# Performance work log

Measured on AMD Instinct MI355X. Metric: run time of the kernel, lower is better.

Reference implementation:

```python
import jax, jax.numpy as jnp
import numpy as np

HUMAN_EXHALATION_FLOW = 0.0052  # ENV_CONFIG.HUMAN_EXHALATION_FLOW
TIME_STEP = 1.0                 # ENV_CONFIG.TIME_STEP
N_NODES = 100_000
N_EDGES = 3_200_000
IN_DIM, OUT_DIM, K = 4, 1, 3
T_HIST = 16


def setup_inputs() -> dict:
    key = jax.random.key(0)
    k1, k2, k3, k4, k5 = jax.random.split(key, 5)
    # columns at [:, -1, :]: 0=concentration, 1=people, 2=size (size divides -> keep away from 0)
    origin_data = jax.random.uniform(k1, (N_NODES, T_HIST, 3), jnp.float32, 0.5, 1.5)
    # raw flow field: conv with kernel K (VALID) maps [E+K-1, K, IN_DIM] -> [E, 1, OUT_DIM]
    flow = jax.random.normal(k2, (N_EDGES + K - 1, K, IN_DIM), jnp.float32)
    edge_index = jax.random.randint(k3, (2, N_EDGES), 0, N_NODES, jnp.int32)
    conv_w = jax.random.normal(k4, (OUT_DIM, IN_DIM, K, K), jnp.float32) * 0.1
    conv_b = jax.random.normal(k5, (OUT_DIM,), jnp.float32) * 0.1
    return {"origin_data": origin_data, "flow": flow, "conv_w": conv_w,
            "conv_b": conv_b, "edge_index": edge_index}


def _flow_conv(flow, conv_w, conv_b):
    # [H, W, C] -> [1, C, H, W] -> conv -> [H', W', out_dim]
    x = jnp.transpose(flow, (2, 0, 1))[None]
    y = jax.lax.conv_general_dilated(
        x, conv_w, window_strides=(1, 1), padding='VALID',
        dimension_numbers=('NCHW', 'OIHW', 'NCHW'))
    y = y + conv_b[None, :, None, None]
    return jnp.transpose(y[0], (1, 2, 0))  # [E, 1, out_dim]


def reference(origin_data, flow, conv_w, conv_b, edge_index):
    concentration = origin_data[:, -1, 0]  # [N]
    people = origin_data[:, -1, 1]         # [N]
    size = origin_data[:, -1, 2]           # [N]
    n = concentration.shape[0]
    mask = jnp.ones((n,), concentration.dtype).at[-1].set(0.0)

    fc = _flow_conv(flow, conv_w, conv_b)  # [E, 1, 1]
    val = fc[:, 0, 0]                      # [E]

    src, dst = edge_index[0], edge_index[1]
    # original loop uses .item() everywhere -> these terms are detached from autodiff
    c_sg = jax.lax.stop_gradient(concentration)
    s_sg = jax.lax.stop_gradient(size)
    v_sg = jax.lax.stop_gradient(val)
    msg = jnp.where(src != dst, v_sg * c_sg[src], 0.0)  # skip self-loops
    node_new = jnp.zeros((n,), concentration.dtype)
    node_new = node_new.at[src].add(-msg / s_sg[src] * TIME_STEP)
    node_new = node_new.at[dst].add(msg / s_sg[dst] * TIME_STEP)

    exhaled = HUMAN_EXHALATION_FLOW * jax.lax.stop_gradient(people) / s_sg  # .item() loop -> detached
    result = concentration + (node_new + exhaled * TIME_STEP) * mask
    out2 = jnp.concatenate([edge_index.T.astype(val.dtype), fc[:, :, 0]], axis=1)  # [E, 3]
    return result[:, None], out2
```

## Files before the change

kernel.cpp:

```cpp
#include <hip/hip_runtime.h>


#define WSH  14
#define WSZ  16384
#define PBF  32

#define OWSH 13
#define OWSZ 8192
#define OPB  16
#define OFPS 8192.0f
#define OQBIAS (1 << 20)
#define OQCLMP ((1 << 19) - 1)

__global__ __launch_bounds__(256) void prep(
    const float* __restrict__ od,
    float* __restrict__ conc,
    unsigned long long* __restrict__ acc,
    int n_nodes)
{
    int n = blockIdx.x * blockDim.x + threadIdx.x;
    if (n >= n_nodes) return;
    conc[n] = od[(long long)n * 48 + 45];
    if (acc) acc[n] = 0ULL;
}

__global__ __launch_bounds__(256) void edge_conv(
    const float* __restrict__ flow, const int* __restrict__ ei,
    const float* __restrict__ conv_w, const float* __restrict__ conv_b,
    const float* __restrict__ conc,
    float* __restrict__ out2, float* __restrict__ bcv, int n_edges)
{
    __shared__ float w[40];
    int t = threadIdx.x;
    if (t < 36) {
        int i  = t & 3;
        int kw = (t >> 2) % 3;
        int kh = t / 12;
        w[t] = conv_w[i * 9 + kh * 3 + kw];
    }
    if (t == 36) w[36] = conv_b[0];
    __syncthreads();

    int e = blockIdx.x * blockDim.x + t;
    if (e >= n_edges) return;

    int s = ei[e];
    int d = ei[n_edges + e];
    float cs = bcv ? conc[s] : 0.0f;

    const float4* fp = (const float4*)(flow + (long long)e * 12);
    float acc = w[36];
#pragma unroll
    for (int q = 0; q < 9; ++q) {
        float4 v = fp[q];
        acc = fmaf(v.x, w[q * 4 + 0], acc);
        acc = fmaf(v.y, w[q * 4 + 1], acc);
        acc = fmaf(v.z, w[q * 4 + 2], acc);
        acc = fmaf(v.w, w[q * 4 + 3], acc);
    }

    float* o = out2 + (long long)e * 3;
    o[0] = (float)s;
    o[1] = (float)d;
    o[2] = acc;
    if (bcv) bcv[e] = acc * cs;
}

__global__ __launch_bounds__(1024) void accum_f(
    const float* __restrict__ out2,
    const float* __restrict__ bcv,
    float* __restrict__ pA,
    float* __restrict__ pB,
    int n_edges, int n_win, int stride)
{
    __shared__ float tA[WSZ];
    __shared__ float tB[WSZ];

    const int xcd = blockIdx.x & 7;
    const int i   = blockIdx.x >> 3;
    const int j   = i / n_win;
    const int sl  = xcd * (PBF >> 3) + j;
    const int w   = i - j * n_win;

    const int t = threadIdx.x;
    for (int k = t; k < WSZ; k += 1024) { tA[k] = 0.f; tB[k] = 0.f; }
    __syncthreads();

    const long long e0 = (long long)sl * n_edges / PBF;
    const long long e1 = (long long)(sl + 1) * n_edges / PBF;

#define PROC(fs, fd, vv, bb)                                          \
    {                                                                  \
        int s_ = (int)(fs), d_ = (int)(fd);                            \
        if (s_ != d_) {                                                \
            if ((s_ >> WSH) == w) atomicAdd(&tA[s_ & (WSZ - 1)], (vv));\
            if ((d_ >> WSH) == w) atomicAdd(&tB[d_ & (WSZ - 1)], (bb));\
        }                                                              \
    }

    long long e = e0 + t;
    for (; e + 3 * 1024 < e1; e += 4 * 1024) {
        const float* r  = out2 + e * 3;
        const float* bb = bcv + e;
        float fs0 = r[0],    fd0 = r[1],    v0 = r[2];
        float fs1 = r[3072], fd1 = r[3073], v1 = r[3074];
        float fs2 = r[6144], fd2 = r[6145], v2 = r[6146];
        float fs3 = r[9216], fd3 = r[9217], v3 = r[9218];
        float b0 = bb[0], b1 = bb[1024], b2 = bb[2048], b3 = bb[3072];
        PROC(fs0, fd0, v0, b0);
        PROC(fs1, fd1, v1, b1);
        PROC(fs2, fd2, v2, b2);
        PROC(fs3, fd3, v3, b3);
    }
    for (; e < e1; e += 1024) {
        const float* r = out2 + e * 3;
        float fs = r[0], fd = r[1], vv = r[2];
        float bb = bcv[e];
        PROC(fs, fd, vv, bb);
    }
#undef PROC
    __syncthreads();

    float* dA = pA + (long long)sl * stride + ((long long)w << WSH);
    float* dB = pB + (long long)sl * stride + ((long long)w << WSH);
    for (int k = t; k < (WSZ >> 2); k += 1024) {
        ((float4*)dA)[k] = ((const float4*)tA)[k];
        ((float4*)dB)[k] = ((const float4*)tB)[k];
    }
}

__global__ __launch_bounds__(256) void node_final_f(
    const float* __restrict__ od,
    const float* __restrict__ conc,
    const float* __restrict__ pA,
    const float* __restrict__ pB,
    float* __restrict__ out, int n_nodes, int stride)
{
    int n = blockIdx.x * blockDim.x + threadIdx.x;
    if (n >= n_nodes) return;

    float a0 = 0.f, a1 = 0.f, a2 = 0.f, a3 = 0.f;
    float b0 = 0.f, b1 = 0.f, b2 = 0.f, b3 = 0.f;
#pragma unroll
    for (int sl = 0; sl < PBF; sl += 4) {
        a0 += pA[(long long)(sl + 0) * stride + n];
        a1 += pA[(long long)(sl + 1) * stride + n];
        a2 += pA[(long long)(sl + 2) * stride + n];
        a3 += pA[(long long)(sl + 3) * stride + n];
        b0 += pB[(long long)(sl + 0) * stride + n];
        b1 += pB[(long long)(sl + 1) * stride + n];
        b2 += pB[(long long)(sl + 2) * stride + n];
        b3 += pB[(long long)(sl + 3) * stride + n];
    }
    float a = (a0 + a1) + (a2 + a3);
    float b = (b0 + b1) + (b2 + b3);

    long long bi = (long long)n * 48 + 45;
    float c  = conc[n];
    float p  = od[bi + 1];
    float is = 1.0f / od[bi + 2];

    float r = c;
    if (n != n_nodes - 1)
        r += (b - a * c) * is + 0.0052f * p * is;
    out[n] = r;
}

__global__ __launch_bounds__(1024) void accum_o(
    const float* __restrict__ out2,
    const float* __restrict__ conc,
    unsigned long long* __restrict__ acc,
    int n_edges, int n_nodes)
{
    __shared__ float tA[OWSZ];
    __shared__ float tB[OWSZ];

    const int w    = blockIdx.x / OPB;
    const int sl   = blockIdx.x % OPB;
    const int base = w << OWSH;

    for (int i = threadIdx.x; i < OWSZ; i += 1024) { tA[i] = 0.f; tB[i] = 0.f; }
    __syncthreads();

    const long long e0 = (long long)sl * n_edges / OPB;
    const long long e1 = (long long)(sl + 1) * n_edges / OPB;
    for (long long e = e0 + threadIdx.x; e < e1; e += 1024) {
        const float* r = out2 + e * 3;
        float fs = r[0], fd = r[1], v = r[2];
        int s = (int)fs, d = (int)fd;
        if (s == d) continue;
        if ((s >> OWSH) == w) atomicAdd(&tA[s - base], v);
        if ((d >> OWSH) == w) atomicAdd(&tB[d - base], v * conc[s]);
    }
    __syncthreads();

    for (int i = threadIdx.x; i < OWSZ; i += 1024) {
        int n = base + i;
        if (n >= n_nodes) continue;
        float a = tA[i], b = tB[i];
        if (a == 0.f && b == 0.f) continue;
        int qa = __float2int_rn(a * OFPS);
        int qb = __float2int_rn(b * OFPS);
        qa = min(max(qa, -OQCLMP), OQCLMP);
        qb = min(max(qb, -OQCLMP), OQCLMP);
        unsigned long long enc =
            ((unsigned long long)(unsigned)(qa + OQBIAS) << 37) +
            ((unsigned long long)(unsigned)(qb + OQBIAS) << 10) + 1ULL;
        atomicAdd(acc + n, enc);
    }
}

__global__ __launch_bounds__(256) void node_final_o(
    const float* __restrict__ od,
    const float* __restrict__ conc,
    const unsigned long long* __restrict__ acc,
    float* __restrict__ out, int n_nodes)
{
    int n = blockIdx.x * blockDim.x + threadIdx.x;
    if (n >= n_nodes) return;

    unsigned long long t = acc[n];
    long long cnt = (long long)(t & 1023ULL);
    unsigned long long t2 = t >> 10;
    long long sbr = (long long)(t2 & ((1ULL << 27) - 1));
    long long sar = (long long)(t2 >> 27);
    float a = (float)(sar - cnt * OQBIAS) * (1.0f / OFPS);
    float b = (float)(sbr - cnt * OQBIAS) * (1.0f / OFPS);

    long long bi = (long long)n * 48 + 45;
    float c  = conc[n];
    float p  = od[bi + 1];
    float is = 1.0f / od[bi + 2];

    float r = c;
    if (n != n_nodes - 1)
        r += (b - a * c) * is + 0.0052f * p * is;
    out[n] = r;
}

extern "C" void kernel_launch(void* const* d_in, const int* in_sizes, int n_in,
                              void* d_out, int out_size, void* d_ws, size_t ws_size,
                              hipStream_t stream) {
    const float* od   = (const float*)d_in[0];
    const float* flow = (const float*)d_in[1];
    const float* cw   = (const float*)d_in[2];
    const float* cb   = (const float*)d_in[3];
    const int*   ei   = (const int*)d_in[4];

    const int n_nodes = in_sizes[0] / 48;
    const int n_edges = in_sizes[4] / 2;

    float* out_res = (float*)d_out;
    float* out2    = out_res + n_nodes;

    dim3 blk(256);
    dim3 grid_nodes((n_nodes + 255) / 256);
    dim3 grid_edges((n_edges + 255) / 256);

    const int n_win  = (n_nodes + WSZ - 1) >> WSH;
    const int stride = n_win << WSH;
    size_t off = 0;
    size_t o_conc = off; off += (((size_t)n_nodes * 4) + 255) & ~255ULL;
    size_t o_bc   = off; off += (((size_t)n_edges * 4) + 255) & ~255ULL;
    size_t o_pA   = off; off += (((size_t)PBF * stride * 4) + 255) & ~255ULL;
    size_t o_pB   = off; off += (((size_t)PBF * stride * 4) + 255) & ~255ULL;
    const bool full = (ws_size >= off);

    float* conc = (float*)((char*)d_ws + o_conc);

    if (full) {
        float* bcv = (float*)((char*)d_ws + o_bc);
        float* pA  = (float*)((char*)d_ws + o_pA);
        float* pB  = (float*)((char*)d_ws + o_pB);

        prep<<<grid_nodes, blk, 0, stream>>>(od, conc, nullptr, n_nodes);
        edge_conv<<<grid_edges, blk, 0, stream>>>(flow, ei, cw, cb, conc,
                                                  out2, bcv, n_edges);
        accum_f<<<dim3(n_win * PBF), dim3(1024), 0, stream>>>(
            out2, bcv, pA, pB, n_edges, n_win, stride);
        node_final_f<<<grid_nodes, blk, 0, stream>>>(od, conc, pA, pB,
                                                     out_res, n_nodes, stride);
    } else {
        unsigned long long* acc =
            (unsigned long long*)((char*)d_ws + (((size_t)n_nodes * 4 + 7) / 8 * 8));
        const int n_win_o = (n_nodes + OWSZ - 1) >> OWSH;

        prep<<<grid_nodes, blk, 0, stream>>>(od, conc, acc, n_nodes);
        edge_conv<<<grid_edges, blk, 0, stream>>>(flow, ei, cw, cb, conc,
                                                  out2, nullptr, n_edges);
        accum_o<<<dim3(n_win_o * OPB), dim3(1024), 0, stream>>>(
            out2, conc, acc, n_edges, n_nodes);
        node_final_o<<<grid_nodes, blk, 0, stream>>>(od, conc, acc,
                                                     out_res, n_nodes);
    }
}
```

Before: 326.3 us.

## Bucket edge contributions by node window before shared-memory accumulation

The edge kernel now computes the conv, then bins each (node, value) pair into per-window record buckets using block-local counters and global tail atomics, with an overflow list. The accumulation kernel reads only its window's bucket instead of scanning every edge once per window, and the partial sums go into smaller 8K windows with 20 slices each. This removes the repeated full-edge reads across windows, at the cost of writing and re-reading 8-byte records, extra atomics, and a larger workspace that could push execution onto the fallback path.

Result: slower. 341.4 us (+4.6%).

```diff
diff --git a/kernel.cpp b/kernel.cpp
--- a/kernel.cpp
+++ b/kernel.cpp
@@ -1,9 +1,11 @@
 #include <hip/hip_runtime.h>
 
 
-#define WSH  14
-#define WSZ  16384
-#define PBF  32
+#define WSH  13
+#define WSZ  8192
+#define SL   20
+#define EPT  4
+#define MAXW 32
 
 #define OWSH 13
 #define OWSZ 8192
@@ -16,19 +18,205 @@
     const float* __restrict__ od,
     float* __restrict__ conc,
     unsigned long long* __restrict__ acc,
+    unsigned* __restrict__ tails,
     int n_nodes)
 {
+    if (blockIdx.x == 0 && tails && threadIdx.x < 65)
+        tails[(size_t)threadIdx.x << 4] = 0u;
     int n = blockIdx.x * blockDim.x + threadIdx.x;
     if (n >= n_nodes) return;
     conc[n] = od[(long long)n * 48 + 45];
     if (acc) acc[n] = 0ULL;
 }
 
-__global__ __launch_bounds__(256) void edge_conv(
+__global__ __launch_bounds__(256) void edge_scatter(
     const float* __restrict__ flow, const int* __restrict__ ei,
     const float* __restrict__ conv_w, const float* __restrict__ conv_b,
     const float* __restrict__ conc,
-    float* __restrict__ out2, float* __restrict__ bcv, int n_edges)
+    float* __restrict__ out2,
+    uint2* __restrict__ recA, uint2* __restrict__ recB,
+    uint2* __restrict__ ovf,
+    unsigned* __restrict__ tails,
+    int n_edges, unsigned cap, unsigned ocap)
+{
+    __shared__ float w[40];
+    __shared__ unsigned cnt[2 * MAXW];
+    __shared__ unsigned bas[2 * MAXW];
+    const int t = threadIdx.x;
+    if (t < 36) {
+        int i  = t & 3;
+        int kw = (t >> 2) % 3;
+        int kh = t / 12;
+        w[t] = conv_w[i * 9 + kh * 3 + kw];
+    }
+    if (t == 36) w[36] = conv_b[0];
+    if (t < 2 * MAXW) cnt[t] = 0u;
+    __syncthreads();
+
+    const long long eb = (long long)blockIdx.x * (256 * EPT) + t;
+    int      sN[EPT], dN[EPT];
+    float    vA[EPT], vB[EPT];
+    unsigned pA_[EPT], pB_[EPT];
+    bool     live[EPT];
+
+#pragma unroll
+    for (int k = 0; k < EPT; ++k) {
+        long long e = eb + (long long)k * 256;
+        live[k] = false;
+        if (e < n_edges) {
+            int s = ei[e];
+            int d = ei[n_edges + e];
+            const float4* fp = (const float4*)(flow + e * 12);
+            float acc = w[36];
+#pragma unroll
+            for (int q = 0; q < 9; ++q) {
+                float4 v = fp[q];
+                acc = fmaf(v.x, w[q * 4 + 0], acc);
+                acc = fmaf(v.y, w[q * 4 + 1], acc);
+                acc = fmaf(v.z, w[q * 4 + 2], acc);
+                acc = fmaf(v.w, w[q * 4 + 3], acc);
+            }
+            float cs = conc[s];
+            float* o = out2 + e * 3;
+            o[0] = (float)s;
+            o[1] = (float)d;
+            o[2] = acc;
+            sN[k] = s; dN[k] = d;
+            vA[k] = acc; vB[k] = acc * cs;
+            if (s != d) {
+                live[k] = true;
+                pA_[k] = atomicAdd(&cnt[(unsigned)s >> WSH], 1u);
+                pB_[k] = atomicAdd(&cnt[MAXW + ((unsigned)d >> WSH)], 1u);
+            }
+        }
+    }
+    __syncthreads();
+    if (t < 2 * MAXW && cnt[t])
+        bas[t] = atomicAdd(&tails[(size_t)t << 4], cnt[t]);
+    __syncthreads();
+
+#pragma unroll
+    for (int k = 0; k < EPT; ++k) {
+        if (!live[k]) continue;
+        {
+            unsigned wa = (unsigned)sN[k] >> WSH;
+            unsigned sa = bas[wa] + pA_[k];
+            uint2 r; r.x = (unsigned)sN[k]; r.y = __float_as_uint(vA[k]);
+            if (sa < cap) {
+                recA[(size_t)wa * cap + sa] = r;
+            } else {
+                unsigned os = atomicAdd(&tails[(size_t)64 << 4], 1u);
+                if (os < ocap) ovf[os] = r;
+            }
+        }
+        {
+            unsigned wb = (unsigned)dN[k] >> WSH;
+            unsigned sb = bas[MAXW + wb] + pB_[k];
+            uint2 r; r.x = (unsigned)dN[k]; r.y = __float_as_uint(vB[k]);
+            if (sb < cap) {
+                recB[(size_t)wb * cap + sb] = r;
+            } else {
+                r.x |= 0x80000000u;
+                unsigned os = atomicAdd(&tails[(size_t)64 << 4], 1u);
+                if (os < ocap) ovf[os] = r;
+            }
+        }
+    }
+}
+
+__global__ __launch_bounds__(1024) void accum_b(
+    const uint2* __restrict__ recA, const uint2* __restrict__ recB,
+    const uint2* __restrict__ ovf,
+    const unsigned* __restrict__ tails,
+    float* __restrict__ pA, float* __restrict__ pB,
+    unsigned cap, unsigned ocap)
+{
+    __shared__ float tA[WSZ];
+    __shared__ float tB[WSZ];
+
+    const int w  = blockIdx.x / SL;
+    const int sl = blockIdx.x % SL;
+    const int t  = threadIdx.x;
+
+    for (int i = t; i < WSZ; i += 1024) { tA[i] = 0.f; tB[i] = 0.f; }
+    __syncthreads();
+
+    {
+        unsigned nA = min(tails[(size_t)w << 4], cap);
+        const uint2* r = recA + (size_t)w * cap;
+        size_t i0 = (size_t)nA * sl / SL, i1 = (size_t)nA * (sl + 1) / SL;
+        for (size_t i = i0 + t; i < i1; i += 1024) {
+            uint2 q = r[i];
+            atomicAdd(&tA[q.x & (WSZ - 1)], __uint_as_float(q.y));
+        }
+    }
+    {
+        unsigned nB = min(tails[(size_t)(MAXW + w) << 4], cap);
+        const uint2* r = recB + (size_t)w * cap;
+        size_t i0 = (size_t)nB * sl / SL, i1 = (size_t)nB * (sl + 1) / SL;
+        for (size_t i = i0 + t; i < i1; i += 1024) {
+            uint2 q = r[i];
+            atomicAdd(&tB[q.x & (WSZ - 1)], __uint_as_float(q.y));
+        }
+    }
+    {
+        unsigned no = min(tails[(size_t)64 << 4], ocap);
+        if (no) {
+            size_t i0 = (size_t)no * sl / SL, i1 = (size_t)no * (sl + 1) / SL;
+            for (size_t i = i0 + t; i < i1; i += 1024) {
+                uint2 q = ovf[i];
+                unsigned node = q.x & 0x7fffffffu;
+                if ((int)(node >> WSH) == w) {
+                    if (q.x >> 31) atomicAdd(&tB[node & (WSZ - 1)], __uint_as_float(q.y));
+                    else           atomicAdd(&tA[node & (WSZ - 1)], __uint_as_float(q.y));
+                }
+            }
+        }
+    }
+    __syncthreads();
+
+    float* dA = pA + ((size_t)blockIdx.x << WSH);
+    float* dB = pB + ((size_t)blockIdx.x << WSH);
+    for (int i = t; i < (WSZ >> 2); i += 1024) {
+        ((float4*)dA)[i] = ((const float4*)tA)[i];
+        ((float4*)dB)[i] = ((const float4*)tB)[i];
+    }
+}
+
+__global__ __launch_bounds__(256) void node_final_b(
+    const float* __restrict__ od,
+    const float* __restrict__ conc,
+    const float* __restrict__ pA,
+    const float* __restrict__ pB,
+    float* __restrict__ out, int n_nodes)
+{
+    int n = blockIdx.x * blockDim.x + threadIdx.x;
+    if (n >= n_nodes) return;
+
+    const int w = n >> WSH, i = n & (WSZ - 1);
+    size_t base = ((size_t)(w * SL) << WSH) + i;
+    float a = 0.f, b = 0.f;
+#pragma unroll
+    for (int sl = 0; sl < SL; ++sl) {
+        a += pA[base + ((size_t)sl << WSH)];
+        b += pB[base + ((size_t)sl << WSH)];
+    }
+
+    long long bi = (long long)n * 48 + 45;
+    float c  = conc[n];
+    float p  = od[bi + 1];
+    float is = 1.0f / od[bi + 2];
+
+    float r = c;
+    if (n != n_nodes - 1)
+        r += (b - a * c) * is + 0.0052f * p * is;
+    out[n] = r;
+}
+
+__global__ __launch_bounds__(256) void edge_conv_o(
+    const float* __restrict__ flow, const int* __restrict__ ei,
+    const float* __restrict__ conv_w, const float* __restrict__ conv_b,
+    float* __restrict__ out2, int n_edges)
 {
     __shared__ float w[40];
     int t = threadIdx.x;
@@ -44,10 +232,6 @@
     int e = blockIdx.x * blockDim.x + t;
     if (e >= n_edges) return;
 
-    int s = ei[e];
-    int d = ei[n_edges + e];
-    float cs = bcv ? conc[s] : 0.0f;
-
     const float4* fp = (const float4*)(flow + (long long)e * 12);
     float acc = w[36];
 #pragma unroll
@@ -60,110 +244,9 @@
     }
 
     float* o = out2 + (long long)e * 3;
-    o[0] = (float)s;
-    o[1] = (float)d;
+    o[0] = (float)ei[e];
+    o[1] = (float)ei[n_edges + e];
     o[2] = acc;
-    if (bcv) bcv[e] = acc * cs;
-}
-
-__global__ __launch_bounds__(1024) void accum_f(
-    const float* __restrict__ out2,
-    const float* __restrict__ bcv,
-    float* __restrict__ pA,
-    float* __restrict__ pB,
-    int n_edges, int n_win, int stride)
-{
-    __shared__ float tA[WSZ];
-    __shared__ float tB[WSZ];
-
-    const int xcd = blockIdx.x & 7;
-    const int i   = blockIdx.x >> 3;
-    const int j   = i / n_win;
-    const int sl  = xcd * (PBF >> 3) + j;
-    const int w   = i - j * n_win;
-
-    const int t = threadIdx.x;
-    for (int k = t; k < WSZ; k += 1024) { tA[k] = 0.f; tB[k] = 0.f; }
-    __syncthreads();
-
-    const long long e0 = (long long)sl * n_edges / PBF;
-    const long long e1 = (long long)(sl + 1) * n_edges / PBF;
-
-#define PROC(fs, fd, vv, bb)                                          \
-    {                                                                  \
-        int s_ = (int)(fs), d_ = (int)(fd);                            \
-        if (s_ != d_) {                                                \
-            if ((s_ >> WSH) == w) atomicAdd(&tA[s_ & (WSZ - 1)], (vv));\
-            if ((d_ >> WSH) == w) atomicAdd(&tB[d_ & (WSZ - 1)], (bb));\
-        }                                                              \
-    }
-
-    long long e = e0 + t;
-    for (; e + 3 * 1024 < e1; e += 4 * 1024) {
-        const float* r  = out2 + e * 3;
-        const float* bb = bcv + e;
-        float fs0 = r[0],    fd0 = r[1],    v0 = r[2];
-        float fs1 = r[3072], fd1 = r[3073], v1 = r[3074];
-        float fs2 = r[6144], fd2 = r[6145], v2 = r[6146];
-        float fs3 = r[9216], fd3 = r[9217], v3 = r[9218];
-        float b0 = bb[0], b1 = bb[1024], b2 = bb[2048], b3 = bb[3072];
-        PROC(fs0, fd0, v0, b0);
-        PROC(fs1, fd1, v1, b1);
-        PROC(fs2, fd2, v2, b2);
-        PROC(fs3, fd3, v3, b3);
-    }
-    for (; e < e1; e += 1024) {
-        const float* r = out2 + e * 3;
-        float fs = r[0], fd = r[1], vv = r[2];
-        float bb = bcv[e];
-        PROC(fs, fd, vv, bb);
-    }
-#undef PROC
-    __syncthreads();
-
-    float* dA = pA + (long long)sl * stride + ((long long)w << WSH);
-    float* dB = pB + (long long)sl * stride + ((long long)w << WSH);
-    for (int k = t; k < (WSZ >> 2); k += 1024) {
-        ((float4*)dA)[k] = ((const float4*)tA)[k];
-        ((float4*)dB)[k] = ((const float4*)tB)[k];
-    }
-}
-
-__global__ __launch_bounds__(256) void node_final_f(
-    const float* __restrict__ od,
-    const float* __restrict__ conc,
-    const float* __restrict__ pA,
-    const float* __restrict__ pB,
-    float* __restrict__ out, int n_nodes, int stride)
-{
-    int n = blockIdx.x * blockDim.x + threadIdx.x;
-    if (n >= n_nodes) return;
-
-    float a0 = 0.f, a1 = 0.f, a2 = 0.f, a3 = 0.f;
-    float b0 = 0.f, b1 = 0.f, b2 = 0.f, b3 = 0.f;
-#pragma unroll
-    for (int sl = 0; sl < PBF; sl += 4) {
-        a0 += pA[(long long)(sl + 0) * stride + n];
-        a1 += pA[(long long)(sl + 1) * stride + n];
-        a2 += pA[(long long)(sl + 2) * stride + n];
-        a3 += pA[(long long)(sl + 3) * stride + n];
-        b0 += pB[(long long)(sl + 0) * stride + n];
-        b1 += pB[(long long)(sl + 1) * stride + n];
-        b2 += pB[(long long)(sl + 2) * stride + n];
-        b3 += pB[(long long)(sl + 3) * stride + n];
-    }
-    float a = (a0 + a1) + (a2 + a3);
-    float b = (b0 + b1) + (b2 + b3);
-
-    long long bi = (long long)n * 48 + 45;
-    float c  = conc[n];
-    float p  = od[bi + 1];
-    float is = 1.0f / od[bi + 2];
-
-    float r = c;
-    if (n != n_nodes - 1)
-        r += (b - a * c) * is + 0.0052f * p * is;
-    out[n] = r;
 }
 
 __global__ __launch_bounds__(1024) void accum_o(
@@ -255,39 +338,50 @@
 
     dim3 blk(256);
     dim3 grid_nodes((n_nodes + 255) / 256);
-    dim3 grid_edges((n_edges + 255) / 256);
-
-    const int n_win  = (n_nodes + WSZ - 1) >> WSH;
-    const int stride = n_win << WSH;
+
+    const int n_win = (n_nodes + WSZ - 1) >> WSH;
+    const unsigned cap  = (unsigned)(n_edges / (n_win > 0 ? n_win : 1))
+                        + (unsigned)(n_edges / 8) + 1024u;
+    const unsigned ocap = (unsigned)(2ULL * (unsigned long long)n_edges);
+
     size_t off = 0;
-    size_t o_conc = off; off += (((size_t)n_nodes * 4) + 255) & ~255ULL;
-    size_t o_bc   = off; off += (((size_t)n_edges * 4) + 255) & ~255ULL;
-    size_t o_pA   = off; off += (((size_t)PBF * stride * 4) + 255) & ~255ULL;
-    size_t o_pB   = off; off += (((size_t)PBF * stride * 4) + 255) & ~255ULL;
-    const bool full = (ws_size >= off);
+    size_t o_conc  = off; off += (((size_t)n_nodes * 4) + 255) & ~255ULL;
+    size_t o_tails = off; off += (65 * 16 * 4 + 255) & ~255ULL;
+    size_t o_recA  = off; off += (((size_t)n_win * cap * 8) + 255) & ~255ULL;
+    size_t o_recB  = off; off += (((size_t)n_win * cap * 8) + 255) & ~255ULL;
+    size_t o_ovf   = off; off += (((size_t)ocap * 8) + 255) & ~255ULL;
+    size_t o_pA    = off; off += (((size_t)n_win * SL * WSZ * 4) + 255) & ~255ULL;
+    size_t o_pB    = off; off += (((size_t)n_win * SL * WSZ * 4) + 255) & ~255ULL;
+    const bool full = (ws_size >= off) && (n_win <= MAXW);
 
     float* conc = (float*)((char*)d_ws + o_conc);
 
     if (full) {
-        float* bcv = (float*)((char*)d_ws + o_bc);
-        float* pA  = (float*)((char*)d_ws + o_pA);
-        float* pB  = (float*)((char*)d_ws + o_pB);
-
-        prep<<<grid_nodes, blk, 0, stream>>>(od, conc, nullptr, n_nodes);
-        edge_conv<<<grid_edges, blk, 0, stream>>>(flow, ei, cw, cb, conc,
-                                                  out2, bcv, n_edges);
-        accum_f<<<dim3(n_win * PBF), dim3(1024), 0, stream>>>(
-            out2, bcv, pA, pB, n_edges, n_win, stride);
-        node_final_f<<<grid_nodes, blk, 0, stream>>>(od, conc, pA, pB,
-                                                     out_res, n_nodes, stride);
+        unsigned* tails = (unsigned*)((char*)d_ws + o_tails);
+        uint2* recA = (uint2*)((char*)d_ws + o_recA);
+        uint2* recB = (uint2*)((char*)d_ws + o_recB);
+        uint2* ovf  = (uint2*)((char*)d_ws + o_ovf);
+        float* pA   = (float*)((char*)d_ws + o_pA);
+        float* pB   = (float*)((char*)d_ws + o_pB);
+
+        dim3 grid_es((n_edges + 256 * EPT - 1) / (256 * EPT));
+
+        prep<<<grid_nodes, blk, 0, stream>>>(od, conc, nullptr, tails, n_nodes);
+        edge_scatter<<<grid_es, blk, 0, stream>>>(flow, ei, cw, cb, conc,
+                                                  out2, recA, recB, ovf, tails,
+                                                  n_edges, cap, ocap);
+        accum_b<<<dim3(n_win * SL), dim3(1024), 0, stream>>>(
+            recA, recB, ovf, tails, pA, pB, cap, ocap);
+        node_final_b<<<grid_nodes, blk, 0, stream>>>(od, conc, pA, pB,
+                                                     out_res, n_nodes);
     } else {
         unsigned long long* acc =
             (unsigned long long*)((char*)d_ws + (((size_t)n_nodes * 4 + 7) / 8 * 8));
         const int n_win_o = (n_nodes + OWSZ - 1) >> OWSH;
-
-        prep<<<grid_nodes, blk, 0, stream>>>(od, conc, acc, n_nodes);
-        edge_conv<<<grid_edges, blk, 0, stream>>>(flow, ei, cw, cb, conc,
-                                                  out2, nullptr, n_edges);
+        dim3 grid_edges((n_edges + 255) / 256);
+
+        prep<<<grid_nodes, blk, 0, stream>>>(od, conc, acc, nullptr, n_nodes);
+        edge_conv_o<<<grid_edges, blk, 0, stream>>>(flow, ei, cw, cb, out2, n_edges);
         accum_o<<<dim3(n_win_o * OPB), dim3(1024), 0, stream>>>(
             out2, conc, acc, n_edges, n_nodes);
         node_final_o<<<grid_nodes, blk, 0, stream>>>(od, conc, acc,
```
